# Kernel optimization log

Measured on AMD Instinct MI355X. Metric: run time of the kernel, lower is better.

## Reference

```python
import jax, jax.numpy as jnp
import numpy as np

B, C, S, L = 8, 512, 2048, 8921


def setup_inputs() -> dict:
    key = jax.random.key(0)
    k1, k2, k3, k4, k5 = jax.random.split(key, 5)
    return {
        "encoded": jax.random.normal(k1, (B, C, S), dtype=jnp.float32),
        "W_attn": jax.random.normal(k2, (L, C), dtype=jnp.float32) * 0.02,
        "b_attn": jax.random.normal(k3, (L,), dtype=jnp.float32) * 0.02,
        "W_cls": jax.random.normal(k4, (L, C), dtype=jnp.float32) * 0.02,
        "b_cls": jax.random.normal(k5, (L,), dtype=jnp.float32) * 0.02,
    }


def reference(encoded, W_attn, b_attn, W_cls, b_cls):
    # encoded: (B, C, S). Linear over channels after transpose -> scores (B, S, L)
    scores = jnp.einsum("bcs,lc->bsl", encoded, W_attn) + b_attn
    # softmax over the sequence dimension (dim=1 of (B, S, L))
    weights = jax.nn.softmax(scores, axis=1)
    # context: (B, L, S) @ (B, S, C) -> (B, L, C)
    context = jnp.einsum("bsl,bcs->blc", weights, encoded)
    # per-label diagonal classifier: elementwise multiply with (L, C) weight, reduce C
    logits = jnp.sum(context * W_cls, axis=2) + b_cls  # (B, L)
    return logits
```

## Files before the change

kernel.cpp:

```cpp
#include <hip/hip_runtime.h>
#include <hip/hip_bf16.h>
#include <stdint.h>

#define B_ 8
#define C_ 512
#define S_ 2048
#define L_ 8921
#define LTILE 128
#define NLT 70
#define BS 128
#define SCHUNK 512
#define NSC 4
#define BK 128
#define ROUNDS 16

#define NW4 ((L_ * C_) / 4)
#define NWBLK ((NW4 + 255) / 256)
#define NEBLK (B_ * 32 * 8)

using f32x4 = __attribute__((ext_vector_type(4))) float;
using s16x8 = __attribute__((ext_vector_type(8))) short;

static __device__ __forceinline__ unsigned short f2bf(float f) {
    union { float f; uint32_t u; } a; a.f = f;
    uint32_t u = a.u;
    return (unsigned short)((u + 0x7fffu + ((u >> 16) & 1u)) >> 16);
}

__global__ void prep(const float* __restrict__ enc, unsigned short* __restrict__ ebt,
                     const float* __restrict__ Wa, unsigned short* __restrict__ waBf,
                     const float* __restrict__ Wc, unsigned short* __restrict__ wcBf) {
    __shared__ float tile[64][65];
    const int x = blockIdx.x;
    const int t = threadIdx.x;

    if (x < NEBLK) {
        int ct = (x & 7) * 64;
        int st = ((x >> 3) & 31) * 64;
        int b  = x >> 8;
        const float* src = enc + (size_t)b * C_ * S_;
        #pragma unroll
        for (int it = 0; it < 16; ++it) {
            int idx = it * 256 + t;
            int rc = idx >> 6, rs = idx & 63;
            tile[rc][rs] = src[(size_t)(ct + rc) * S_ + st + rs];
        }
        __syncthreads();
        unsigned short* dst = ebt + (size_t)b * S_ * C_;
        #pragma unroll
        for (int it = 0; it < 4; ++it) {
            int idx = it * 256 + t;
            int rs  = idx >> 4;
            int rc4 = (idx & 15) << 2;
            ushort4 o;
            o.x = f2bf(tile[rc4 + 0][rs]);
            o.y = f2bf(tile[rc4 + 1][rs]);
            o.z = f2bf(tile[rc4 + 2][rs]);
            o.w = f2bf(tile[rc4 + 3][rs]);
            *(ushort4*)(dst + (size_t)(st + rs) * C_ + ct + rc4) = o;
        }
    } else {
        int wb = x - NEBLK;
        const float* src;
        unsigned short* dst;
        if (wb < NWBLK) { src = Wa; dst = waBf; }
        else            { src = Wc; dst = wcBf; wb -= NWBLK; }
        int i = wb * 256 + t;
        if (i < NW4) {
            float4 v = ((const float4*)src)[i];
            ushort4 o;
            o.x = f2bf(v.x); o.y = f2bf(v.y); o.z = f2bf(v.z); o.w = f2bf(v.w);
            ((ushort4*)dst)[i] = o;
        }
    }
}

__global__ __launch_bounds__(256, 2) void attn_main(
    const unsigned short* __restrict__ ebt,
    const unsigned short* __restrict__ wa,
    const unsigned short* __restrict__ wc,
    float* __restrict__ pnum, float* __restrict__ pden)
{
    __shared__ __align__(16) unsigned char sE[65536];

    const int tid  = threadIdx.x;
    const int lane = tid & 63;
    const int wave = tid >> 6;

    const int x  = blockIdx.x;
    const int lt = x >> 5;
    const int rb = x & 31;
    const int b  = rb >> 2;
    const int sc = rb & 3;
    const int l0 = lt * LTILE;

    if ((x >> 8) & 1) asm volatile("s_sleep 48");

    int rowOff[2];
    #pragma unroll
    for (int mf = 0; mf < 2; ++mf) {
        int gl = l0 + wave * 32 + mf * 16 + (lane & 15);
        if (gl > L_ - 1) gl = L_ - 1;
        rowOff[mf] = gl * C_ + ((lane >> 4) << 3);
    }

    const size_t ebase = (size_t)b * S_ * C_;
    const int kgsrcE = (((lane & 7) ^ ((lane >> 3) & 7)) << 3);
    const int rowPart = (lane & 15) << 7;
    const int laneQ = lane >> 4;
    const int laneX = lane & 7;

    struct W4 { s16x8 a0, a1, c0, c1; };
    auto loadW = [&](int rr, int ks) -> W4 {
        const int co = ((rr & 3) << 7) + (ks << 5);
        W4 w;
        w.a0 = *(const s16x8*)(wa + rowOff[0] + co);
        w.a1 = *(const s16x8*)(wa + rowOff[1] + co);
        w.c0 = *(const s16x8*)(wc + rowOff[0] + co);
        w.c1 = *(const s16x8*)(wc + rowOff[1] + co);
        return w;
    };

    auto stageE = [&](int rr2) {
        const int kcol = (rr2 & 3) << 7;
        const int sBase = sc * SCHUNK + ((rr2 >> 2) << 7);
        unsigned char* dbase = sE + ((rr2 & 1) << 15);
        #pragma unroll
        for (int jj = 0; jj < 8; ++jj) {
            const int idx = wave * 8 + jj;
            const int h   = idx >> 4;
            const int j   = idx & 15;
            const int sg  = sBase + j * 8 + (lane >> 3);
            const unsigned short* g = ebt + ebase + (size_t)sg * C_
                                      + kcol + (h << 6) + kgsrcE;
            __builtin_amdgcn_global_load_lds(
                (__attribute__((address_space(1))) void*)g,
                (__attribute__((address_space(3))) void*)(dbase + (h << 14) + j * 1024),
                16, 0, 0);
        }
    };

    f32x4 accS[2][8], accV[2][8];
    #pragma unroll
    for (int mf = 0; mf < 2; ++mf)
        #pragma unroll
        for (int nf = 0; nf < 8; ++nf) {
            accS[mf][nf] = (f32x4){0.f, 0.f, 0.f, 0.f};
            accV[mf][nf] = (f32x4){0.f, 0.f, 0.f, 0.f};
        }
    float numAcc[2][4], denAcc[2][4];
    #pragma unroll
    for (int mf = 0; mf < 2; ++mf)
        #pragma unroll
        for (int r = 0; r < 4; ++r) { numAcc[mf][r] = 0.f; denAcc[mf][r] = 0.f; }

    stageE(0);
    W4 wcur = loadW(0, 0);
    asm volatile("s_waitcnt vmcnt(0)" ::: "memory");
    __builtin_amdgcn_s_barrier();
    __builtin_amdgcn_sched_barrier(0);

    for (int rr = 0; rr < ROUNDS; ++rr) {
        if (rr + 1 < ROUNDS) stageE(rr + 1);
        __builtin_amdgcn_sched_barrier(0);

        const unsigned char* fb = sE + ((rr & 1) << 15);

        #pragma unroll
        for (int ks = 0; ks < 4; ++ks) {
            W4 wnxt;
            if (ks < 3)                wnxt = loadW(rr, ks + 1);
            else if (rr + 1 < ROUNDS)  wnxt = loadW(rr + 1, 0);
            else                       wnxt = wcur;

            const unsigned char* fbh = fb + ((ks >> 1) << 14);
            const int chunkX = ((((ks & 1) << 2) + laneQ) ^ laneX) << 4;

            s16x8 fe[8];
            #pragma unroll
            for (int nf = 0; nf < 8; ++nf)
                fe[nf] = *(const s16x8*)(fbh + (nf << 11) + rowPart + chunkX);

            __builtin_amdgcn_s_setprio(1);
            #pragma unroll
            for (int nf = 0; nf < 8; ++nf) {
                accS[0][nf] = __builtin_amdgcn_mfma_f32_16x16x32_bf16(wcur.a0, fe[nf], accS[0][nf], 0, 0, 0);
                accS[1][nf] = __builtin_amdgcn_mfma_f32_16x16x32_bf16(wcur.a1, fe[nf], accS[1][nf], 0, 0, 0);
                accV[0][nf] = __builtin_amdgcn_mfma_f32_16x16x32_bf16(wcur.c0, fe[nf], accV[0][nf], 0, 0, 0);
                accV[1][nf] = __builtin_amdgcn_mfma_f32_16x16x32_bf16(wcur.c1, fe[nf], accV[1][nf], 0, 0, 0);
            }
            __builtin_amdgcn_s_setprio(0);
            wcur = wnxt;
        }

        if ((rr & 3) == 3) {
            #pragma unroll
            for (int mf = 0; mf < 2; ++mf)
                #pragma unroll
                for (int nf = 0; nf < 8; ++nf)
                    #pragma unroll
                    for (int r = 0; r < 4; ++r) {
                        float e = __expf(accS[mf][nf][r]);
                        denAcc[mf][r] += e;
                        numAcc[mf][r] += e * accV[mf][nf][r];
                        accS[mf][nf][r] = 0.f;
                        accV[mf][nf][r] = 0.f;
                    }
        }

        __builtin_amdgcn_sched_barrier(0);
        asm volatile("s_waitcnt vmcnt(4)" ::: "memory");
        __builtin_amdgcn_s_barrier();
        __builtin_amdgcn_sched_barrier(0);
    }

    const size_t obase = ((size_t)((b * NLT + lt) * NSC + sc)) * LTILE;
    #pragma unroll
    for (int mf = 0; mf < 2; ++mf)
        #pragma unroll
        for (int r = 0; r < 4; ++r) {
            float n = numAcc[mf][r], d = denAcc[mf][r];
            n += __shfl_xor(n, 1);  d += __shfl_xor(d, 1);
            n += __shfl_xor(n, 2);  d += __shfl_xor(d, 2);
            n += __shfl_xor(n, 4);  d += __shfl_xor(d, 4);
            n += __shfl_xor(n, 8);  d += __shfl_xor(d, 8);
            if ((lane & 15) == 0) {
                int row = wave * 32 + mf * 16 + (lane >> 4) * 4 + r;
                pnum[obase + row] = n;
                pden[obase + row] = d;
            }
        }
}

__global__ void finalize(const float* __restrict__ pnum, const float* __restrict__ pden,
                         const float* __restrict__ bcls, float* __restrict__ out) {
    int gid = blockIdx.x * 256 + threadIdx.x;
    if (gid >= B_ * L_) return;
    int b = gid / L_, l = gid - b * L_;
    int lt = l >> 7, row = l & 127;
    float n = 0.f, d = 0.f;
    #pragma unroll
    for (int s = 0; s < NSC; ++s) {
        size_t idx = ((size_t)((b * NLT + lt) * NSC + s)) * LTILE + row;
        n += pnum[idx];
        d += pden[idx];
    }
    out[gid] = n / d + bcls[l];
}

extern "C" void kernel_launch(void* const* d_in, const int* in_sizes, int n_in,
                              void* d_out, int out_size, void* d_ws, size_t ws_size,
                              hipStream_t stream) {
    (void)in_sizes; (void)n_in; (void)out_size; (void)ws_size;
    const float* enc  = (const float*)d_in[0];
    const float* Wa   = (const float*)d_in[1];
    const float* Wc   = (const float*)d_in[3];
    const float* bcls = (const float*)d_in[4];

    unsigned char* ws = (unsigned char*)d_ws;
    const size_t oEbt = 0;
    const size_t oWa  = oEbt + 16777216;
    const size_t oWc  = oWa + 9136128;
    const size_t oPn  = oWc + 9136128;
    const size_t oPd  = oPn + 1146880;

    unsigned short* ebt  = (unsigned short*)(ws + oEbt);
    unsigned short* waBf = (unsigned short*)(ws + oWa);
    unsigned short* wcBf = (unsigned short*)(ws + oWc);
    float* pnum = (float*)(ws + oPn);
    float* pden = (float*)(ws + oPd);

    prep<<<NEBLK + 2 * NWBLK, 256, 0, stream>>>(enc, ebt, Wa, waBf, Wc, wcBf);
    attn_main<<<NLT * 32, 256, 0, stream>>>(ebt, waBf, wcBf, pnum, pden);
    finalize<<<(B_ * L_ + 255) / 256, 256, 0, stream>>>(pnum, pden, bcls, (float*)d_out);
}
```

Before: 411.8 us.

## Load encoded tiles straight from global memory instead of staging through LDS

Removes the double-buffered LDS staging of the encoded operand, along with its barriers and the staggered s_sleep. Each wave now loads its MFMA B-fragments directly from global memory (relying on L1/L2), with a schedule barrier after each k-step. This drops LDS traffic and workgroup synchronisation. In exchange, every wave issues redundant global loads for the same encoded data and exposes global latency without prefetch overlap.

```diff
diff --git a/kernel.cpp b/kernel.cpp
--- a/kernel.cpp
+++ b/kernel.cpp
@@ -81,8 +81,6 @@
     const unsigned short* __restrict__ wc,
     float* __restrict__ pnum, float* __restrict__ pden)
 {
-    __shared__ __align__(16) unsigned char sE[65536];
-
     const int tid  = threadIdx.x;
     const int lane = tid & 63;
     const int wave = tid >> 6;
@@ -94,8 +92,6 @@
     const int sc = rb & 3;
     const int l0 = lt * LTILE;
 
-    if ((x >> 8) & 1) asm volatile("s_sleep 48");
-
     int rowOff[2];
     #pragma unroll
     for (int mf = 0; mf < 2; ++mf) {
@@ -104,11 +100,8 @@
         rowOff[mf] = gl * C_ + ((lane >> 4) << 3);
     }
 
-    const size_t ebase = (size_t)b * S_ * C_;
-    const int kgsrcE = (((lane & 7) ^ ((lane >> 3) & 7)) << 3);
-    const int rowPart = (lane & 15) << 7;
-    const int laneQ = lane >> 4;
-    const int laneX = lane & 7;
+    const unsigned short* feP = ebt + (size_t)b * S_ * C_
+        + (size_t)(sc * SCHUNK + (lane & 15)) * C_ + ((lane >> 4) << 3);
 
     struct W4 { s16x8 a0, a1, c0, c1; };
     auto loadW = [&](int rr, int ks) -> W4 {
@@ -121,25 +114,6 @@
         return w;
     };
 
-    auto stageE = [&](int rr2) {
-        const int kcol = (rr2 & 3) << 7;
-        const int sBase = sc * SCHUNK + ((rr2 >> 2) << 7);
-        unsigned char* dbase = sE + ((rr2 & 1) << 15);
-        #pragma unroll
-        for (int jj = 0; jj < 8; ++jj) {
-            const int idx = wave * 8 + jj;
-            const int h   = idx >> 4;
-            const int j   = idx & 15;
-            const int sg  = sBase + j * 8 + (lane >> 3);
-            const unsigned short* g = ebt + ebase + (size_t)sg * C_
-                                      + kcol + (h << 6) + kgsrcE;
-            __builtin_amdgcn_global_load_lds(
-                (__attribute__((address_space(1))) void*)g,
-                (__attribute__((address_space(3))) void*)(dbase + (h << 14) + j * 1024),
-                16, 0, 0);
-        }
-    };
-
     f32x4 accS[2][8], accV[2][8];
     #pragma unroll
     for (int mf = 0; mf < 2; ++mf)
@@ -154,17 +128,10 @@
         #pragma unroll
         for (int r = 0; r < 4; ++r) { numAcc[mf][r] = 0.f; denAcc[mf][r] = 0.f; }
 
-    stageE(0);
     W4 wcur = loadW(0, 0);
-    asm volatile("s_waitcnt vmcnt(0)" ::: "memory");
-    __builtin_amdgcn_s_barrier();
-    __builtin_amdgcn_sched_barrier(0);
 
     for (int rr = 0; rr < ROUNDS; ++rr) {
-        if (rr + 1 < ROUNDS) stageE(rr + 1);
-        __builtin_amdgcn_sched_barrier(0);
-
-        const unsigned char* fb = sE + ((rr & 1) << 15);
+        const int eOff = ((rr >> 2) << 16) + ((rr & 3) << 7);
 
         #pragma unroll
         for (int ks = 0; ks < 4; ++ks) {
@@ -173,13 +140,10 @@
             else if (rr + 1 < ROUNDS)  wnxt = loadW(rr + 1, 0);
             else                       wnxt = wcur;
 
-            const unsigned char* fbh = fb + ((ks >> 1) << 14);
-            const int chunkX = ((((ks & 1) << 2) + laneQ) ^ laneX) << 4;
-
             s16x8 fe[8];
             #pragma unroll
             for (int nf = 0; nf < 8; ++nf)
-                fe[nf] = *(const s16x8*)(fbh + (nf << 11) + rowPart + chunkX);
+                fe[nf] = *(const s16x8*)(feP + eOff + nf * 8192 + ks * 32);
 
             __builtin_amdgcn_s_setprio(1);
             #pragma unroll
@@ -191,6 +155,7 @@
             }
             __builtin_amdgcn_s_setprio(0);
             wcur = wnxt;
+            __builtin_amdgcn_sched_barrier(0);
         }
 
         if ((rr & 3) == 3) {
@@ -207,11 +172,6 @@
                         accV[mf][nf][r] = 0.f;
                     }
         }
-
-        __builtin_amdgcn_sched_barrier(0);
-        asm volatile("s_waitcnt vmcnt(4)" ::: "memory");
-        __builtin_amdgcn_s_barrier();
-        __builtin_amdgcn_sched_barrier(0);
     }
 
     const size_t obase = ((size_t)((b * NLT + lt) * NSC + sc)) * LTILE;
```

Measured after the change: 984.2 us. +139.0%, slower.

## Split waves into score and value roles with LDS exchange of exp weights

Applied to the files above, without the earlier changes.

Each block now covers 64 labels instead of 128, and waves specialize: two waves compute attention scores (W_attn) and two compute value projections (W_cls) for the same label rows. The score waves exponentiate, convert the weights to bf16 and write them to LDS, and the value waves fold them into the numerator one 8-round period later. This halves per-wave accumulator registers so occupancy can rise to 3 blocks per CU, with smaller LDS and K-steps of 64. The cost is twice as many blocks re-staging the encoded tile, bf16 rounding of the exp weights, extra LDS traffic, and the removal of the s_sleep stagger.

```diff
diff --git a/kernel.cpp b/kernel.cpp
--- a/kernel.cpp
+++ b/kernel.cpp
@@ -6,13 +6,13 @@
 #define C_ 512
 #define S_ 2048
 #define L_ 8921
-#define LTILE 128
-#define NLT 70
+#define LTILE 64
+#define NLT 140
 #define BS 128
 #define SCHUNK 512
 #define NSC 4
-#define BK 128
-#define ROUNDS 16
+#define BK 64
+#define ROUNDS 32
 
 #define NW4 ((L_ * C_) / 4)
 #define NWBLK ((NW4 + 255) / 256)
@@ -25,6 +25,9 @@
     union { float f; uint32_t u; } a; a.f = f;
     uint32_t u = a.u;
     return (unsigned short)((u + 0x7fffu + ((u >> 16) & 1u)) >> 16);
+}
+static __device__ __forceinline__ float bf2f(uint32_t h16) {
+    union { uint32_t u; float f; } a; a.u = h16 << 16; return a.f;
 }
 
 __global__ void prep(const float* __restrict__ enc, unsigned short* __restrict__ ebt,
@@ -75,17 +78,19 @@
     }
 }
 
-__global__ __launch_bounds__(256, 2) void attn_main(
+__global__ __launch_bounds__(256, 3) void attn_main(
     const unsigned short* __restrict__ ebt,
     const unsigned short* __restrict__ wa,
     const unsigned short* __restrict__ wc,
     float* __restrict__ pnum, float* __restrict__ pden)
 {
-    __shared__ __align__(16) unsigned char sE[65536];
+    __shared__ __align__(16) unsigned char sE[49152];
 
     const int tid  = threadIdx.x;
     const int lane = tid & 63;
     const int wave = tid >> 6;
+    const int h    = wave & 1;
+    const int isV  = wave >> 1;
 
     const int x  = blockIdx.x;
     const int lt = x >> 5;
@@ -94,68 +99,83 @@
     const int sc = rb & 3;
     const int l0 = lt * LTILE;
 
-    if ((x >> 8) & 1) asm volatile("s_sleep 48");
-
     int rowOff[2];
     #pragma unroll
     for (int mf = 0; mf < 2; ++mf) {
-        int gl = l0 + wave * 32 + mf * 16 + (lane & 15);
+        int gl = l0 + h * 32 + mf * 16 + (lane & 15);
         if (gl > L_ - 1) gl = L_ - 1;
         rowOff[mf] = gl * C_ + ((lane >> 4) << 3);
     }
+    const unsigned short* wsel = isV ? wc : wa;
 
     const size_t ebase = (size_t)b * S_ * C_;
     const int kgsrcE = (((lane & 7) ^ ((lane >> 3) & 7)) << 3);
     const int rowPart = (lane & 15) << 7;
     const int laneQ = lane >> 4;
     const int laneX = lane & 7;
-
-    struct W4 { s16x8 a0, a1, c0, c1; };
-    auto loadW = [&](int rr, int ks) -> W4 {
-        const int co = ((rr & 3) << 7) + (ks << 5);
-        W4 w;
-        w.a0 = *(const s16x8*)(wa + rowOff[0] + co);
-        w.a1 = *(const s16x8*)(wa + rowOff[1] + co);
-        w.c0 = *(const s16x8*)(wc + rowOff[0] + co);
-        w.c1 = *(const s16x8*)(wc + rowOff[1] + co);
+    const int ebufB = 32768 + (h << 13);
+
+    struct W2 { s16x8 r0, r1; };
+    auto loadW = [&](int rr, int k) -> W2 {
+        const int co = ((rr & 7) << 6) + (k << 5);
+        W2 w;
+        w.r0 = *(const s16x8*)(wsel + rowOff[0] + co);
+        w.r1 = *(const s16x8*)(wsel + rowOff[1] + co);
         return w;
     };
 
     auto stageE = [&](int rr2) {
-        const int kcol = (rr2 & 3) << 7;
-        const int sBase = sc * SCHUNK + ((rr2 >> 2) << 7);
-        unsigned char* dbase = sE + ((rr2 & 1) << 15);
-        #pragma unroll
-        for (int jj = 0; jj < 8; ++jj) {
-            const int idx = wave * 8 + jj;
-            const int h   = idx >> 4;
-            const int j   = idx & 15;
-            const int sg  = sBase + j * 8 + (lane >> 3);
-            const unsigned short* g = ebt + ebase + (size_t)sg * C_
-                                      + kcol + (h << 6) + kgsrcE;
+        const int kcol = (rr2 & 7) << 6;
+        const int sBase = sc * SCHUNK + ((rr2 >> 3) << 7);
+        unsigned char* dbase = sE + ((rr2 & 1) << 14);
+        #pragma unroll
+        for (int jj = 0; jj < 4; ++jj) {
+            const int j = wave * 4 + jj;
+            const int sg = sBase + j * 8 + (lane >> 3);
+            const unsigned short* g = ebt + ebase + (size_t)sg * C_ + kcol + kgsrcE;
             __builtin_amdgcn_global_load_lds(
                 (__attribute__((address_space(1))) void*)g,
-                (__attribute__((address_space(3))) void*)(dbase + (h << 14) + j * 1024),
+                (__attribute__((address_space(3))) void*)(dbase + j * 1024),
                 16, 0, 0);
         }
     };
 
-    f32x4 accS[2][8], accV[2][8];
+    f32x4 acc[2][8];
     #pragma unroll
     for (int mf = 0; mf < 2; ++mf)
         #pragma unroll
-        for (int nf = 0; nf < 8; ++nf) {
-            accS[mf][nf] = (f32x4){0.f, 0.f, 0.f, 0.f};
-            accV[mf][nf] = (f32x4){0.f, 0.f, 0.f, 0.f};
-        }
-    float numAcc[2][4], denAcc[2][4];
+        for (int nf = 0; nf < 8; ++nf)
+            acc[mf][nf] = (f32x4){0.f, 0.f, 0.f, 0.f};
+    float redAcc[2][4];
     #pragma unroll
     for (int mf = 0; mf < 2; ++mf)
         #pragma unroll
-        for (int r = 0; r < 4; ++r) { numAcc[mf][r] = 0.f; denAcc[mf][r] = 0.f; }
+        for (int r = 0; r < 4; ++r) redAcc[mf][r] = 0.f;
+
+    auto vFold = [&]() {
+        #pragma unroll
+        for (int j = 0; j < 8; ++j) {
+            uint4 q = *(const uint4*)(sE + ebufB + (lane << 7) + ((j ^ (lane & 7)) << 4));
+            uint32_t wd[4] = {q.x, q.y, q.z, q.w};
+            #pragma unroll
+            for (int w2 = 0; w2 < 4; ++w2) {
+                const int v0 = j * 8 + w2 * 2, v1 = v0 + 1;
+                float e0 = bf2f(wd[w2] & 0xffffu);
+                float e1 = bf2f(wd[w2] >> 16);
+                redAcc[v0 >> 5][v0 & 3] += e0 * acc[v0 >> 5][(v0 >> 2) & 7][v0 & 3];
+                redAcc[v1 >> 5][v1 & 3] += e1 * acc[v1 >> 5][(v1 >> 2) & 7][v1 & 3];
+            }
+        }
+        #pragma unroll
+        for (int mf = 0; mf < 2; ++mf)
+            #pragma unroll
+            for (int nf = 0; nf < 8; ++nf)
+                #pragma unroll
+                for (int r = 0; r < 4; ++r) acc[mf][nf][r] = 0.f;
+    };
 
     stageE(0);
-    W4 wcur = loadW(0, 0);
+    W2 wcur = loadW(0, 0);
     asm volatile("s_waitcnt vmcnt(0)" ::: "memory");
     __builtin_amdgcn_s_barrier();
     __builtin_amdgcn_sched_barrier(0);
@@ -164,70 +184,86 @@
         if (rr + 1 < ROUNDS) stageE(rr + 1);
         __builtin_amdgcn_sched_barrier(0);
 
-        const unsigned char* fb = sE + ((rr & 1) << 15);
-
-        #pragma unroll
-        for (int ks = 0; ks < 4; ++ks) {
-            W4 wnxt;
-            if (ks < 3)                wnxt = loadW(rr, ks + 1);
-            else if (rr + 1 < ROUNDS)  wnxt = loadW(rr + 1, 0);
-            else                       wnxt = wcur;
-
-            const unsigned char* fbh = fb + ((ks >> 1) << 14);
-            const int chunkX = ((((ks & 1) << 2) + laneQ) ^ laneX) << 4;
-
+        if (isV && (rr & 7) == 0 && rr > 0) vFold();
+
+        const unsigned char* fb = sE + ((rr & 1) << 14);
+        {
+            W2 wn = loadW(rr, 1);
             s16x8 fe[8];
             #pragma unroll
             for (int nf = 0; nf < 8; ++nf)
-                fe[nf] = *(const s16x8*)(fbh + (nf << 11) + rowPart + chunkX);
-
+                fe[nf] = *(const s16x8*)(fb + (nf << 11) + rowPart + (((laneQ) ^ laneX) << 4));
             __builtin_amdgcn_s_setprio(1);
             #pragma unroll
             for (int nf = 0; nf < 8; ++nf) {
-                accS[0][nf] = __builtin_amdgcn_mfma_f32_16x16x32_bf16(wcur.a0, fe[nf], accS[0][nf], 0, 0, 0);
-                accS[1][nf] = __builtin_amdgcn_mfma_f32_16x16x32_bf16(wcur.a1, fe[nf], accS[1][nf], 0, 0, 0);
-                accV[0][nf] = __builtin_amdgcn_mfma_f32_16x16x32_bf16(wcur.c0, fe[nf], accV[0][nf], 0, 0, 0);
-                accV[1][nf] = __builtin_amdgcn_mfma_f32_16x16x32_bf16(wcur.c1, fe[nf], accV[1][nf], 0, 0, 0);
+                acc[0][nf] = __builtin_amdgcn_mfma_f32_16x16x32_bf16(wcur.r0, fe[nf], acc[0][nf], 0, 0, 0);
+                acc[1][nf] = __builtin_amdgcn_mfma_f32_16x16x32_bf16(wcur.r1, fe[nf], acc[1][nf], 0, 0, 0);
             }
             __builtin_amdgcn_s_setprio(0);
-            wcur = wnxt;
-        }
-
-        if ((rr & 3) == 3) {
+            wcur = wn;
+        }
+        {
+            W2 wn = (rr + 1 < ROUNDS) ? loadW(rr + 1, 0) : wcur;
+            s16x8 fe[8];
+            #pragma unroll
+            for (int nf = 0; nf < 8; ++nf)
+                fe[nf] = *(const s16x8*)(fb + (nf << 11) + rowPart + (((4 + laneQ) ^ laneX) << 4));
+            __builtin_amdgcn_s_setprio(1);
+            #pragma unroll
+            for (int nf = 0; nf < 8; ++nf) {
+                acc[0][nf] = __builtin_amdgcn_mfma_f32_16x16x32_bf16(wcur.r0, fe[nf], acc[0][nf], 0, 0, 0);
+                acc[1][nf] = __builtin_amdgcn_mfma_f32_16x16x32_bf16(wcur.r1, fe[nf], acc[1][nf], 0, 0, 0);
+            }
+            __builtin_amdgcn_s_setprio(0);
+            wcur = wn;
+        }
+
+        if (!isV && (rr & 7) == 7) {
+            #pragma unroll
+            for (int j = 0; j < 8; ++j) {
+                uint32_t wd[4];
+                #pragma unroll
+                for (int w2 = 0; w2 < 4; ++w2) {
+                    const int v0 = j * 8 + w2 * 2, v1 = v0 + 1;
+                    float e0 = __expf(acc[v0 >> 5][(v0 >> 2) & 7][v0 & 3]);
+                    float e1 = __expf(acc[v1 >> 5][(v1 >> 2) & 7][v1 & 3]);
+                    redAcc[v0 >> 5][v0 & 3] += e0;
+                    redAcc[v1 >> 5][v1 & 3] += e1;
+                    wd[w2] = (uint32_t)f2bf(e0) | ((uint32_t)f2bf(e1) << 16);
+                }
+                *(uint4*)(sE + ebufB + (lane << 7) + ((j ^ (lane & 7)) << 4)) =
+                    make_uint4(wd[0], wd[1], wd[2], wd[3]);
+            }
             #pragma unroll
             for (int mf = 0; mf < 2; ++mf)
                 #pragma unroll
                 for (int nf = 0; nf < 8; ++nf)
                     #pragma unroll
-                    for (int r = 0; r < 4; ++r) {
-                        float e = __expf(accS[mf][nf][r]);
-                        denAcc[mf][r] += e;
-                        numAcc[mf][r] += e * accV[mf][nf][r];
-                        accS[mf][nf][r] = 0.f;
-                        accV[mf][nf][r] = 0.f;
-                    }
+                    for (int r = 0; r < 4; ++r) acc[mf][nf][r] = 0.f;
         }
 
         __builtin_amdgcn_sched_barrier(0);
-        asm volatile("s_waitcnt vmcnt(4)" ::: "memory");
+        asm volatile("s_waitcnt vmcnt(2) lgkmcnt(0)" ::: "memory");
         __builtin_amdgcn_s_barrier();
         __builtin_amdgcn_sched_barrier(0);
     }
 
+    if (isV) vFold();
+
     const size_t obase = ((size_t)((b * NLT + lt) * NSC + sc)) * LTILE;
+    float* dst = isV ? pnum : pden;
     #pragma unroll
     for (int mf = 0; mf < 2; ++mf)
         #pragma unroll
         for (int r = 0; r < 4; ++r) {
-            float n = numAcc[mf][r], d = denAcc[mf][r];
-            n += __shfl_xor(n, 1);  d += __shfl_xor(d, 1);
-            n += __shfl_xor(n, 2);  d += __shfl_xor(d, 2);
-            n += __shfl_xor(n, 4);  d += __shfl_xor(d, 4);
-            n += __shfl_xor(n, 8);  d += __shfl_xor(d, 8);
+            float v = redAcc[mf][r];
+            v += __shfl_xor(v, 1);
+            v += __shfl_xor(v, 2);
+            v += __shfl_xor(v, 4);
+            v += __shfl_xor(v, 8);
             if ((lane & 15) == 0) {
-                int row = wave * 32 + mf * 16 + (lane >> 4) * 4 + r;
-                pnum[obase + row] = n;
-                pden[obase + row] = d;
+                int row = h * 32 + mf * 16 + (lane >> 4) * 4 + r;
+                dst[obase + row] = v;
             }
         }
 }
@@ -237,7 +273,7 @@
     int gid = blockIdx.x * 256 + threadIdx.x;
     if (gid >= B_ * L_) return;
     int b = gid / L_, l = gid - b * L_;
-    int lt = l >> 7, row = l & 127;
+    int lt = l >> 6, row = l & 63;
     float n = 0.f, d = 0.f;
     #pragma unroll
     for (int s = 0; s < NSC; ++s) {
```

After: 454.3 us. +10.3%, slower.

## Double label tile to 256 with 512-thread blocks and 4-stage K pipeline

Applied to the files above, without the earlier changes.

Doubles the label tile per block (LTILE 256, 8 waves), so each staged tile of encoded activations in LDS feeds twice as many label rows and global reloads of E drop. The K step per round shrinks to 64, and LDS becomes a 4-buffer ring with three stages prefetched ahead, using graded vmcnt waits. The s_sleep staggering is removed. The risk is register pressure: with 512 threads and 2 blocks per CU, the large accumulator set may spill or limit occupancy.

```diff
diff --git a/kernel.cpp b/kernel.cpp
--- a/kernel.cpp
+++ b/kernel.cpp
@@ -6,13 +6,13 @@
 #define C_ 512
 #define S_ 2048
 #define L_ 8921
-#define LTILE 128
-#define NLT 70
+#define LTILE 256
+#define NLT 35
 #define BS 128
 #define SCHUNK 512
 #define NSC 4
-#define BK 128
-#define ROUNDS 16
+#define BK 64
+#define ROUNDS 32
 
 #define NW4 ((L_ * C_) / 4)
 #define NWBLK ((NW4 + 255) / 256)
@@ -75,7 +75,7 @@
     }
 }
 
-__global__ __launch_bounds__(256, 2) void attn_main(
+__global__ __launch_bounds__(512, 2) void attn_main(
     const unsigned short* __restrict__ ebt,
     const unsigned short* __restrict__ wa,
     const unsigned short* __restrict__ wc,
@@ -94,8 +94,6 @@
     const int sc = rb & 3;
     const int l0 = lt * LTILE;
 
-    if ((x >> 8) & 1) asm volatile("s_sleep 48");
-
     int rowOff[2];
     #pragma unroll
     for (int mf = 0; mf < 2; ++mf) {
@@ -111,8 +109,8 @@
     const int laneX = lane & 7;
 
     struct W4 { s16x8 a0, a1, c0, c1; };
-    auto loadW = [&](int rr, int ks) -> W4 {
-        const int co = ((rr & 3) << 7) + (ks << 5);
+    auto loadW = [&](int rr, int k) -> W4 {
+        const int co = ((rr & 7) << 6) + (k << 5);
         W4 w;
         w.a0 = *(const s16x8*)(wa + rowOff[0] + co);
         w.a1 = *(const s16x8*)(wa + rowOff[1] + co);
@@ -122,20 +120,17 @@
     };
 
     auto stageE = [&](int rr2) {
-        const int kcol = (rr2 & 3) << 7;
-        const int sBase = sc * SCHUNK + ((rr2 >> 2) << 7);
-        unsigned char* dbase = sE + ((rr2 & 1) << 15);
-        #pragma unroll
-        for (int jj = 0; jj < 8; ++jj) {
-            const int idx = wave * 8 + jj;
-            const int h   = idx >> 4;
-            const int j   = idx & 15;
-            const int sg  = sBase + j * 8 + (lane >> 3);
-            const unsigned short* g = ebt + ebase + (size_t)sg * C_
-                                      + kcol + (h << 6) + kgsrcE;
+        const int kcol = (rr2 & 7) << 6;
+        const int sBase = sc * SCHUNK + ((rr2 >> 3) << 7);
+        unsigned char* dbase = sE + ((rr2 & 3) << 14);
+        #pragma unroll
+        for (int jj = 0; jj < 2; ++jj) {
+            const int j = wave * 2 + jj;
+            const int sg = sBase + j * 8 + (lane >> 3);
+            const unsigned short* g = ebt + ebase + (size_t)sg * C_ + kcol + kgsrcE;
             __builtin_amdgcn_global_load_lds(
                 (__attribute__((address_space(1))) void*)g,
-                (__attribute__((address_space(3))) void*)(dbase + (h << 14) + j * 1024),
+                (__attribute__((address_space(3))) void*)(dbase + j * 1024),
                 16, 0, 0);
         }
     };
@@ -155,32 +150,22 @@
         for (int r = 0; r < 4; ++r) { numAcc[mf][r] = 0.f; denAcc[mf][r] = 0.f; }
 
     stageE(0);
+    stageE(1);
+    stageE(2);
     W4 wcur = loadW(0, 0);
     asm volatile("s_waitcnt vmcnt(0)" ::: "memory");
     __builtin_amdgcn_s_barrier();
     __builtin_amdgcn_sched_barrier(0);
 
     for (int rr = 0; rr < ROUNDS; ++rr) {
-        if (rr + 1 < ROUNDS) stageE(rr + 1);
-        __builtin_amdgcn_sched_barrier(0);
-
-        const unsigned char* fb = sE + ((rr & 1) << 15);
-
-        #pragma unroll
-        for (int ks = 0; ks < 4; ++ks) {
-            W4 wnxt;
-            if (ks < 3)                wnxt = loadW(rr, ks + 1);
-            else if (rr + 1 < ROUNDS)  wnxt = loadW(rr + 1, 0);
-            else                       wnxt = wcur;
-
-            const unsigned char* fbh = fb + ((ks >> 1) << 14);
-            const int chunkX = ((((ks & 1) << 2) + laneQ) ^ laneX) << 4;
-
+        const unsigned char* fb = sE + ((rr & 3) << 14);
+
+        {
+            W4 wnxt = loadW(rr, 1);
             s16x8 fe[8];
             #pragma unroll
             for (int nf = 0; nf < 8; ++nf)
-                fe[nf] = *(const s16x8*)(fbh + (nf << 11) + rowPart + chunkX);
-
+                fe[nf] = *(const s16x8*)(fb + (nf << 11) + rowPart + (((laneQ) ^ laneX) << 4));
             __builtin_amdgcn_s_setprio(1);
             #pragma unroll
             for (int nf = 0; nf < 8; ++nf) {
@@ -192,8 +177,25 @@
             __builtin_amdgcn_s_setprio(0);
             wcur = wnxt;
         }
-
-        if ((rr & 3) == 3) {
+        {
+            W4 wfut = (rr + 1 < ROUNDS) ? loadW(rr + 1, 0) : wcur;
+            s16x8 fe[8];
+            #pragma unroll
+            for (int nf = 0; nf < 8; ++nf)
+                fe[nf] = *(const s16x8*)(fb + (nf << 11) + rowPart + (((4 + laneQ) ^ laneX) << 4));
+            __builtin_amdgcn_s_setprio(1);
+            #pragma unroll
+            for (int nf = 0; nf < 8; ++nf) {
+                accS[0][nf] = __builtin_amdgcn_mfma_f32_16x16x32_bf16(wcur.a0, fe[nf], accS[0][nf], 0, 0, 0);
+                accS[1][nf] = __builtin_amdgcn_mfma_f32_16x16x32_bf16(wcur.a1, fe[nf], accS[1][nf], 0, 0, 0);
+                accV[0][nf] = __builtin_amdgcn_mfma_f32_16x16x32_bf16(wcur.c0, fe[nf], accV[0][nf], 0, 0, 0);
+                accV[1][nf] = __builtin_amdgcn_mfma_f32_16x16x32_bf16(wcur.c1, fe[nf], accV[1][nf], 0, 0, 0);
+            }
+            __builtin_amdgcn_s_setprio(0);
+            wcur = wfut;
+        }
+
+        if ((rr & 7) == 7) {
             #pragma unroll
             for (int mf = 0; mf < 2; ++mf)
                 #pragma unroll
@@ -208,10 +210,15 @@
                     }
         }
 
+        if (rr + 3 < ROUNDS) stageE(rr + 3);
         __builtin_amdgcn_sched_barrier(0);
-        asm volatile("s_waitcnt vmcnt(4)" ::: "memory");
-        __builtin_amdgcn_s_barrier();
-        __builtin_amdgcn_sched_barrier(0);
+        if (rr + 1 < ROUNDS) {
+            if (rr + 3 < ROUNDS)      asm volatile("s_waitcnt vmcnt(8)" ::: "memory");
+            else if (rr + 2 < ROUNDS) asm volatile("s_waitcnt vmcnt(6)" ::: "memory");
+            else                      asm volatile("s_waitcnt vmcnt(4)" ::: "memory");
+            __builtin_amdgcn_s_barrier();
+            __builtin_amdgcn_sched_barrier(0);
+        }
     }
 
     const size_t obase = ((size_t)((b * NLT + lt) * NSC + sc)) * LTILE;
@@ -237,7 +244,7 @@
     int gid = blockIdx.x * 256 + threadIdx.x;
     if (gid >= B_ * L_) return;
     int b = gid / L_, l = gid - b * L_;
-    int lt = l >> 7, row = l & 127;
+    int lt = l >> 8, row = l & 255;
     float n = 0.f, d = 0.f;
     #pragma unroll
     for (int s = 0; s < NSC; ++s) {
@@ -271,6 +278,6 @@
     float* pden = (float*)(ws + oPd);
 
     prep<<<NEBLK + 2 * NWBLK, 256, 0, stream>>>(enc, ebt, Wa, waBf, Wc, wcBf);
-    attn_main<<<NLT * 32, 256, 0, stream>>>(ebt, waBf, wcBf, pnum, pden);
+    attn_main<<<NLT * 32, 512, 0, stream>>>(ebt, waBf, wcBf, pnum, pden);
     finalize<<<(B_ * L_ + 255) / 256, 256, 0, stream>>>(pnum, pden, bcls, (float*)d_out);
 }
```

Measured after the change: 446.5 us. +8.4%, slower.
